# Performance work log

Hardware: AMD Instinct MI355X
Metric: run time of the kernel (lower is better)

## Reference

```python
import jax, jax.numpy as jnp
from jax import lax
import numpy as np

T, B, S, D, H, NC = 10, 16, 200, 768, 300, 4


def setup_inputs() -> dict:
    key = jax.random.key(0)
    ks = jax.random.split(key, 20)
    f = lambda k, shp: jax.random.normal(k, shp, dtype=jnp.float32)
    u = lambda k, shp: jax.random.uniform(k, shp, dtype=jnp.float32)
    return {
        "input_ids": jax.random.randint(ks[0], (B, T, 16), 0, 50265),
        "sequence_list": f(ks[1], (T, B, S, D)),
        "start_probs": u(ks[2], (T, B, S)),
        "end_probs": u(ks[3], (T, B, S)),
        "classification_probs": u(ks[4], (T, B, NC)),
        "before_state_start_probs": u(ks[5], (T, B, S)),
        "before_state_end_probs": u(ks[6], (T, B, S)),
        "before_state_classification_probs": u(ks[7], (T, B, NC)),
        "unk_mask": u(ks[8], (B, T, S)),
        "none_mask": u(ks[9], (B, T, S)),
        "ans_mask": u(ks[10], (B, T, S)),
        "Wih_f": f(ks[11], (4 * H, 5 * D)) * 0.02,
        "Whh_f": f(ks[12], (4 * H, H)) * 0.02,
        "bih_f": jnp.zeros((4 * H,), jnp.float32),
        "bhh_f": jnp.zeros((4 * H,), jnp.float32),
        "Wih_b": f(ks[13], (4 * H, 5 * D)) * 0.02,
        "Whh_b": f(ks[14], (4 * H, H)) * 0.02,
        "bih_b": jnp.zeros((4 * H,), jnp.float32),
        "bhh_b": jnp.zeros((4 * H,), jnp.float32),
        "Wcls": f(ks[15], (NC, S * 2 * H)) * 0.005,
        "bcls": jnp.zeros((NC,), jnp.float32),
    }


def _attn_weight(p, c, am, um, nm):
    # p: [B,S] probs; c: [B,NC] class probs; masks [B,S]
    # sum of three masked weighted copies collapses to one fused weight
    return p * (am * c[:, 0:1] + um * c[:, 1:2] + nm * c[:, 2:3])


def _lstm_dir(zx, Whh, bhh, h0, c0):
    # zx: [S,B,4H] precomputed x @ Wih.T + bih (big GEMM outside the scan)
    def step(carry, zt):
        h, c = carry
        z = zt + h @ Whh.T + bhh
        i, f, g, o = jnp.split(z, 4, axis=-1)  # torch gate order i,f,g,o
        c = jax.nn.sigmoid(f) * c + jax.nn.sigmoid(i) * jnp.tanh(g)
        h = jax.nn.sigmoid(o) * jnp.tanh(c)
        return (h, c), h
    (h, c), ys = lax.scan(step, (h0, c0), zx)
    return ys, h, c


def reference(input_ids, sequence_list, start_probs, end_probs, classification_probs,
              before_state_start_probs, before_state_end_probs, before_state_classification_probs,
              unk_mask, none_mask, ans_mask,
              Wih_f, Whh_f, bih_f, bhh_f, Wih_b, Whh_b, bih_b, bhh_b, Wcls, bcls):
    T_, B_, S_ = start_probs.shape
    H_ = Whh_f.shape[-1]
    amT = jnp.swapaxes(ans_mask, 0, 1)   # [T,B,S]
    umT = jnp.swapaxes(unk_mask, 0, 1)
    nmT = jnp.swapaxes(none_mask, 0, 1)
    # before-state attention (only step 0's probs are used, per the original code)
    bss = _attn_weight(before_state_start_probs[0], before_state_classification_probs[0],
                       amT[0], umT[0], nmT[0])[..., None] * sequence_list[0]
    bse = _attn_weight(before_state_end_probs[0], before_state_classification_probs[0],
                       amT[0], umT[0], nmT[0])[..., None] * sequence_list[0]
    z0 = jnp.zeros((B_, H_), start_probs.dtype)

    def outer(carry, xs):
        prev_s, prev_e, hf, cf, hb, cb = carry
        sp, ep, cp, am, um, nm, seq = xs
        s_att = _attn_weight(sp, cp, am, um, nm)[..., None] * seq  # [B,S,D]
        e_att = _attn_weight(ep, cp, am, um, nm)[..., None] * seq
        rnn_in = jnp.concatenate([seq, s_att, e_att, prev_s, prev_e], axis=-1)  # [B,S,5D]
        xT = jnp.swapaxes(rnn_in, 0, 1)  # [S,B,5D]
        zf = xT @ Wih_f.T + bih_f        # [S,B,4H]
        zb = xT[::-1] @ Wih_b.T + bih_b
        yf, hf, cf = _lstm_dir(zf, Whh_f, bhh_f, hf, cf)
        yb, hb, cb = _lstm_dir(zb, Whh_b, bhh_b, hb, cb)
        y = jnp.concatenate([yf, yb[::-1]], axis=-1)            # [S,B,2H]
        y = jnp.swapaxes(y, 0, 1).reshape(B_, -1)               # [B,S*2H]
        logits = jax.nn.relu(y) @ Wcls.T + bcls                 # [B,NC]
        return (s_att, e_att, hf, cf, hb, cb), logits

    init = (bss, bse, z0, z0, z0, z0)
    xs = (start_probs, end_probs, classification_probs, amT, umT, nmT, sequence_list)
    _, logits = lax.scan(outer, init, xs)
    return logits  # [T,B,NC]
```

## Files before the change

kernel.cpp:

```cpp
#include <hip/hip_runtime.h>
#include <stdint.h>
#include <stdio.h>

#define T_ 10
#define B_ 16
#define S_ 200
#define D_ 768
#define H_ 300
#define NC_ 4
#define M_ (S_ * B_)
#define K5_ (5 * D_)
#define N2_ 2400
#define G4_ 1200
#define HXW_SLOT 4864
#define HLDS_STRIDE 336

typedef unsigned short u16;
typedef unsigned int u32;
typedef __attribute__((ext_vector_type(8))) short short8;
typedef __attribute__((ext_vector_type(4))) float float4v;

static __device__ __forceinline__ u16 f2bf(float x) {
  union { float f; u32 u; } v; v.f = x;
  u32 u = v.u;
  u32 r = (u + 0x7FFFu + ((u >> 16) & 1u)) >> 16;
  return (u16)r;
}

static __device__ __forceinline__ void async16(const void* g, void* l) {
  __builtin_amdgcn_global_load_lds((const __attribute__((address_space(1))) u32*)g,
                                   (__attribute__((address_space(3))) u32*)l, 16, 0, 0);
}

static __device__ __forceinline__ float sigmoid_f(float x) {
  return 1.f / (1.f + __expf(-x));
}
static __device__ __forceinline__ float tanh_f(float x) {
  float e = __expf(2.f * x);
  return 1.f - 2.f / (e + 1.f);
}

__global__ void k_prep_s(const float* __restrict__ seq,
                         const float* __restrict__ sp, const float* __restrict__ ep,
                         const float* __restrict__ cp,
                         const float* __restrict__ bsp, const float* __restrict__ bep,
                         const float* __restrict__ bcp,
                         const float* __restrict__ um, const float* __restrict__ nm,
                         const float* __restrict__ am,
                         u16* __restrict__ s0, u16* __restrict__ sa, u16* __restrict__ sb,
                         u16* __restrict__ sa0, u16* __restrict__ sb0) {
  int bid = blockIdx.x;
  int tid = threadIdx.x;
  if (bid < T_ * M_) {
    int t = bid / M_;
    int r = bid % M_;
    int s = r >> 4, b = r & 15;
    float c0 = cp[(t * B_ + b) * NC_ + 0];
    float c1 = cp[(t * B_ + b) * NC_ + 1];
    float c2 = cp[(t * B_ + b) * NC_ + 2];
    int mi = (b * T_ + t) * S_ + s;
    float w = am[mi] * c0 + um[mi] * c1 + nm[mi] * c2;
    float aw = sp[(t * B_ + b) * S_ + s] * w;
    float bw = ep[(t * B_ + b) * S_ + s] * w;
    const float* x = seq + ((size_t)(t * B_ + b) * S_ + s) * D_;
    size_t ob = (size_t)bid * D_;
    for (int d = tid; d < D_; d += 256) {
      float xv = x[d];
      s0[ob + d] = f2bf(xv);
      sa[ob + d] = f2bf(aw * xv);
      sb[ob + d] = f2bf(bw * xv);
    }
  } else {
    int r = bid - T_ * M_;
    int s = r >> 4, b = r & 15;
    float c0 = bcp[b * NC_ + 0], c1 = bcp[b * NC_ + 1], c2 = bcp[b * NC_ + 2];
    int mi = (b * T_ + 0) * S_ + s;
    float w = am[mi] * c0 + um[mi] * c1 + nm[mi] * c2;
    float aw = bsp[b * S_ + s] * w;
    float bw = bep[b * S_ + s] * w;
    const float* x = seq + ((size_t)b * S_ + s) * D_;
    size_t ob = (size_t)r * D_;
    for (int d = tid; d < D_; d += 256) {
      float xv = x[d];
      sa0[ob + d] = f2bf(aw * xv);
      sb0[ob + d] = f2bf(bw * xv);
    }
  }
}

__global__ void k_prep_w(const float* __restrict__ wf, const float* __restrict__ wb,
                         const float* __restrict__ whf, const float* __restrict__ whb,
                         const float* __restrict__ bihf, const float* __restrict__ bhhf,
                         const float* __restrict__ bihb, const float* __restrict__ bhhb,
                         const float* __restrict__ bcls,
                         u16* __restrict__ wcat, u16* __restrict__ whh,
                         float* __restrict__ bias, float* __restrict__ outp,
                         u32* __restrict__ hxw) {
  int bid = blockIdx.x, tid = threadIdx.x;
  if (bid < N2_) {
    const float* src = bid < G4_ ? wf + (size_t)bid * K5_ : wb + (size_t)(bid - G4_) * K5_;
    u16* dst = wcat + (size_t)bid * K5_;
    for (int k = tid; k < K5_; k += 256) dst[k] = f2bf(src[k]);
  } else if (bid < N2_ + 2 * G4_) {
    int r = bid - N2_;
    int dir = r / G4_, n = r % G4_;
    const float* src = (dir ? whb : whf) + (size_t)n * H_;
    u16* dst = whh + (size_t)(dir * G4_ + n) * 320;
    for (int k = tid; k < 320; k += 256) dst[k] = (k < H_) ? f2bf(src[k]) : (u16)0;
  } else {
    for (int i = tid; i < 2 * G4_; i += 256) {
      int dir = i / G4_, n = i % G4_;
      bias[i] = dir ? (bihb[n] + bhhb[n]) : (bihf[n] + bhhf[n]);
    }
    for (int i = tid; i < T_ * B_ * NC_; i += 256) outp[i] = bcls[i & 3];
    for (int i = tid; i < 2 * 2 * HXW_SLOT; i += 256) hxw[i] = 0;
  }
}

__global__ __launch_bounds__(256, 3) void k_gemm(
    const u16* __restrict__ s0, const u16* __restrict__ sa, const u16* __restrict__ sb,
    const u16* __restrict__ sa0, const u16* __restrict__ sb0,
    const u16* __restrict__ wcat, float* __restrict__ z, int t) {
  __shared__ __align__(16) u16 As[128 * 32];
  __shared__ __align__(16) u16 Bs[128 * 32];
  int m0 = blockIdx.x * 128;
  int n0 = blockIdx.y * 128;
  int tid = threadIdx.x;
  int lane = tid & 63, wv = tid >> 6;
  int wm = wv & 1, wn = wv >> 1;

  const u16* ap[5];
  ap[0] = s0 + (size_t)t * M_ * D_;
  ap[1] = sa + (size_t)t * M_ * D_;
  ap[2] = sb + (size_t)t * M_ * D_;
  ap[3] = t ? sa + (size_t)(t - 1) * M_ * D_ : sa0;
  ap[4] = t ? sb + (size_t)(t - 1) * M_ * D_ : sb0;

  float4v acc[4][4];
#pragma unroll
  for (int i = 0; i < 4; i++)
#pragma unroll
    for (int j = 0; j < 4; j++) acc[i][j] = (float4v){0.f, 0.f, 0.f, 0.f};

  int rowA = tid >> 2;
  int seg = tid & 3;

  for (int which = 0; which < 5; ++which) {
    const u16* ab = which == 0 ? ap[0] : which == 1 ? ap[1] : which == 2 ? ap[2]
                    : which == 3 ? ap[3] : ap[4];
    for (int kk = 0; kk < 24; ++kk) {
      int kof = kk * 32;
#pragma unroll
      for (int j = 0; j < 2; ++j) {
        int row = j * 64 + rowA;
        const u16* g = ab + (size_t)(m0 + row) * D_ + kof + seg * 8;
        async16(g, As + wv * 512 + j * 2048);
      }
#pragma unroll
      for (int j = 0; j < 2; ++j) {
        int row = j * 64 + rowA;
        int nr = n0 + row;
        if (nr > N2_ - 1) nr = N2_ - 1;
        const u16* g = wcat + (size_t)nr * K5_ + which * D_ + kof + seg * 8;
        async16(g, Bs + wv * 512 + j * 2048);
      }
      __syncthreads();
      short8 af[4], bf[4];
#pragma unroll
      for (int i = 0; i < 4; i++) {
        af[i] = *(const short8*)&As[(wm * 64 + i * 16 + (lane & 15)) * 32 + (lane >> 4) * 8];
        bf[i] = *(const short8*)&Bs[(wn * 64 + i * 16 + (lane & 15)) * 32 + (lane >> 4) * 8];
      }
#pragma unroll
      for (int i = 0; i < 4; i++)
#pragma unroll
        for (int j = 0; j < 4; j++)
          acc[i][j] = __builtin_amdgcn_mfma_f32_16x16x32_bf16(af[i], bf[j], acc[i][j], 0, 0, 0);
      __syncthreads();
    }
  }
#pragma unroll
  for (int i = 0; i < 4; i++) {
    int m = m0 + wm * 64 + i * 16 + (lane >> 4) * 4;
#pragma unroll
    for (int j = 0; j < 4; j++) {
      int n = n0 + wn * 64 + j * 16 + (lane & 15);
      if (n < N2_) {
#pragma unroll
        for (int r = 0; r < 4; r++) z[(size_t)(m + r) * N2_ + n] = acc[i][j][r];
      }
    }
  }
}

__global__ __launch_bounds__(1024, 4) void k_lstm(
    const float* __restrict__ z, const u16* __restrict__ whh,
    const float* __restrict__ bias, const float* __restrict__ wcls,
    u32* __restrict__ hxw, float* __restrict__ outp,
    float* __restrict__ cst, int t) {
  __shared__ __align__(16) u16 h_lds[16 * HLDS_STRIDE];
  __shared__ __align__(16) float smem[4160];

  int wgid = blockIdx.x;
  int dir = wgid / 5;
  int w = wgid % 5;
  int tid = threadIdx.x;
  int lane = tid & 63, wv = tid >> 6;
  int gate = wv >> 2, q = wv & 3;

  short8 bfr[10];
  {
    int col = lane & 15;
    int u = w * 64 + q * 16 + col;
    int krow = (lane >> 4) * 8;
    if (u < H_) {
      const u16* base = whh + (size_t)(dir * G4_ + gate * H_ + u) * 320 + krow;
#pragma unroll
      for (int kk = 0; kk < 10; ++kk) bfr[kk] = *(const short8*)(base + kk * 32);
    } else {
#pragma unroll
      for (int kk = 0; kk < 10; ++kk) bfr[kk] = (short8){0, 0, 0, 0, 0, 0, 0, 0};
    }
  }

  int b = tid >> 6;
  int u_loc = tid & 63;
  int u_glob = w * 64 + u_loc;
  bool active = u_glob < H_;
  float bias_r[4];
#pragma unroll
  for (int g = 0; g < 4; ++g)
    bias_r[g] = active ? bias[dir * G4_ + g * H_ + u_glob] : 0.f;

  float c_state = t > 0 ? cst[wgid * 1024 + tid] : 0.f;
  float clsacc[4] = {0.f, 0.f, 0.f, 0.f};

  for (int i = tid; i < 16 * HLDS_STRIDE; i += 1024) h_lds[i] = 0;
  __syncthreads();

  u32* hx_base = hxw + dir * 2 * HXW_SLOT;

  u32 pend0 = 0, pendA = 0;
  int widx[5], lofs[5];
#pragma unroll
  for (int j = 0; j < 5; ++j) {
    int i = tid + j * 1024;
    widx[j] = i;
    lofs[j] = 0;
    if (i < 16 * 304) {
      int bb = i / 304;
      int uu = i - bb * 304;
      if (uu < H_) {
        lofs[j] = bb * HLDS_STRIDE + uu;
        pendA |= 1u << j;
        if (!(uu >= w * 64 && uu < (w + 1) * 64)) pend0 |= 1u << j;
      }
    }
  }

  for (int s_mod = 0; s_mod < S_; ++s_mod) {
    int g = t * S_ + s_mod;
    int s_in = dir ? (S_ - 1 - s_mod) : s_mod;

    float z_in[4] = {0.f, 0.f, 0.f, 0.f}, wc[4] = {0.f, 0.f, 0.f, 0.f};
    if (active) {
      const float* zr = z + (size_t)(s_in * B_ + b) * N2_ + dir * G4_;
      int ycol = s_in * 600 + dir * H_ + u_glob;
#pragma unroll
      for (int gg = 0; gg < 4; ++gg) z_in[gg] = zr[gg * H_ + u_glob];
#pragma unroll
      for (int n = 0; n < 4; ++n) wc[n] = wcls[(size_t)n * (S_ * 600) + ycol];
    }

    if (g > 0) {
      const u32* src = hx_base + (g & 1) * HXW_SLOT;
      u32 pend = (s_mod == 0) ? pendA : pend0;
      int tries = 0;
      while (pend && tries < (1 << 20)) {
        u32 got[5];
#pragma unroll
        for (int j = 0; j < 5; ++j)
          if (pend & (1u << j))
            got[j] = __hip_atomic_load(&src[widx[j]], __ATOMIC_RELAXED,
                                       __HIP_MEMORY_SCOPE_AGENT);
#pragma unroll
        for (int j = 0; j < 5; ++j)
          if ((pend & (1u << j)) && (got[j] >> 16) >= (u32)g) {
            h_lds[lofs[j]] = (u16)(got[j] & 0xffffu);
            pend &= ~(1u << j);
          }
        ++tries;
      }
      __syncthreads();
    }

    {
      float4v acc = (float4v){0.f, 0.f, 0.f, 0.f};
      int m = lane & 15;
      int kbase = (lane >> 4) * 8;
      const u16* hl = h_lds + m * HLDS_STRIDE + kbase;
#pragma unroll
      for (int kk = 0; kk < 10; ++kk) {
        short8 af = *(const short8*)(hl + kk * 32);
        acc = __builtin_amdgcn_mfma_f32_16x16x32_bf16(af, bfr[kk], acc, 0, 0, 0);
      }
      int col = lane & 15;
      int rb = (lane >> 4) * 4;
#pragma unroll
      for (int r = 0; r < 4; r++)
        smem[(gate * 16 + rb + r) * 65 + q * 16 + col] = acc[r];
    }
    __syncthreads();

    if (active) {
      float zi = smem[(0 * 16 + b) * 65 + u_loc] + z_in[0] + bias_r[0];
      float zf = smem[(1 * 16 + b) * 65 + u_loc] + z_in[1] + bias_r[1];
      float zg = smem[(2 * 16 + b) * 65 + u_loc] + z_in[2] + bias_r[2];
      float zo = smem[(3 * 16 + b) * 65 + u_loc] + z_in[3] + bias_r[3];
      float ig = sigmoid_f(zi);
      float fg = sigmoid_f(zf);
      float gg = tanh_f(zg);
      float og = sigmoid_f(zo);
      c_state = fg * c_state + ig * gg;
      float hval = og * tanh_f(c_state);
      u16 hb = f2bf(hval);
      u32 wrd = ((u32)(g + 1) << 16) | (u32)hb;
      __hip_atomic_store(&hx_base[((g + 1) & 1) * HXW_SLOT + b * 304 + u_glob], wrd,
                         __ATOMIC_RELAXED, __HIP_MEMORY_SCOPE_AGENT);
      h_lds[b * HLDS_STRIDE + u_glob] = hb;
      float rv = hval > 0.f ? hval : 0.f;
#pragma unroll
      for (int n = 0; n < 4; ++n) clsacc[n] += rv * wc[n];
    }

    if (s_mod == S_ - 1) {
      __syncthreads();
#pragma unroll
      for (int n = 0; n < 4; ++n) smem[(b * 64 + u_loc) * 4 + n] = clsacc[n];
      __syncthreads();
      if (tid < B_ * NC_) {
        int bb = tid >> 2, n = tid & 3;
        float s = 0.f;
        for (int u = 0; u < 64; ++u) s += smem[(bb * 64 + u) * 4 + n];
        atomicAdd(&outp[(t * B_ + bb) * NC_ + n], s);
      }
    }
  }
  cst[wgid * 1024 + tid] = c_state;
}

extern "C" void kernel_launch(void* const* d_in, const int* in_sizes, int n_in,
                              void* d_out, int out_size, void* d_ws, size_t ws_size,
                              hipStream_t stream) {
  const float* seq = (const float*)d_in[1];
  const float* sp = (const float*)d_in[2];
  const float* ep = (const float*)d_in[3];
  const float* cp = (const float*)d_in[4];
  const float* bsp = (const float*)d_in[5];
  const float* bep = (const float*)d_in[6];
  const float* bcp = (const float*)d_in[7];
  const float* um = (const float*)d_in[8];
  const float* nm = (const float*)d_in[9];
  const float* am = (const float*)d_in[10];
  const float* wihf = (const float*)d_in[11];
  const float* whhf = (const float*)d_in[12];
  const float* bihf = (const float*)d_in[13];
  const float* bhhf = (const float*)d_in[14];
  const float* wihb = (const float*)d_in[15];
  const float* whhb = (const float*)d_in[16];
  const float* bihb = (const float*)d_in[17];
  const float* bhhb = (const float*)d_in[18];
  const float* wcls = (const float*)d_in[19];
  const float* bcls = (const float*)d_in[20];

  char* ws = (char*)d_ws;
  size_t off = 0;
  auto alloc = [&](size_t bytes) -> char* {
    char* p = ws + off;
    off += (bytes + 255) & ~(size_t)255;
    return p;
  };
  u16* S0 = (u16*)alloc((size_t)T_ * M_ * D_ * 2);
  u16* SA = (u16*)alloc((size_t)T_ * M_ * D_ * 2);
  u16* SB = (u16*)alloc((size_t)T_ * M_ * D_ * 2);
  u16* SA0 = (u16*)alloc((size_t)M_ * D_ * 2);
  u16* SB0 = (u16*)alloc((size_t)M_ * D_ * 2);
  u16* WCAT = (u16*)alloc((size_t)N2_ * K5_ * 2);
  u16* WHH = (u16*)alloc((size_t)2 * G4_ * 320 * 2);
  float* BIAS = (float*)alloc((size_t)2 * G4_ * 4);
  float* Z = (float*)alloc((size_t)M_ * N2_ * 4);
  u32* HXW = (u32*)alloc((size_t)2 * 2 * HXW_SLOT * 4);
  float* CST = (float*)alloc((size_t)10 * 1024 * 4);

  if (off > ws_size) {
    fprintf(stderr, "[kernel] ws too small: need %zu, have %zu\n", off, ws_size);
    return;
  }

  hipLaunchKernelGGL(k_prep_s, dim3(T_ * M_ + M_), dim3(256), 0, stream,
                     seq, sp, ep, cp, bsp, bep, bcp, um, nm, am, S0, SA, SB, SA0, SB0);
  hipLaunchKernelGGL(k_prep_w, dim3(N2_ + 2 * G4_ + 1), dim3(256), 0, stream,
                     wihf, wihb, whhf, whhb, bihf, bhhf, bihb, bhhb, bcls,
                     WCAT, WHH, BIAS, (float*)d_out, HXW);
  for (int t = 0; t < T_; ++t) {
    hipLaunchKernelGGL(k_gemm, dim3(25, 19, 1), dim3(256), 0, stream,
                       S0, SA, SB, SA0, SB0, WCAT, Z, t);
    hipLaunchKernelGGL(k_lstm, dim3(10), dim3(1024), 0, stream,
                       Z, WHH, BIAS, wcls, HXW, (float*)d_out, CST, t);
  }
}
```

Baseline: 6.793 ms.

## Overlap next-step input GEMM with current LSTM recurrence in one fused launch

Merges the GEMM and LSTM kernels into one launch. The first 10 blocks run the recurrent LSTM for step t while the remaining 130 blocks compute the input projection GEMM for step t+1 into a double-buffered Z. The GEMM tile grows to 256x256 with 1024 threads. The LSTM polling loop now uses wide dwordx4 loads, and the h LDS stride is padded. This aims to hide the GEMM behind the latency-bound recurrence, at the cost of larger tiles and lower GEMM occupancy, and the GEMM blocks compete for bandwidth with the spinning LSTM blocks.

```diff
diff --git a/kernel.cpp b/kernel.cpp
--- a/kernel.cpp
+++ b/kernel.cpp
@@ -13,12 +13,13 @@
 #define N2_ 2400
 #define G4_ 1200
 #define HXW_SLOT 4864
-#define HLDS_STRIDE 336
+#define HLDS_STRIDE 344
 
 typedef unsigned short u16;
 typedef unsigned int u32;
 typedef __attribute__((ext_vector_type(8))) short short8;
 typedef __attribute__((ext_vector_type(4))) float float4v;
+typedef __attribute__((ext_vector_type(4))) unsigned int u32x4;
 
 static __device__ __forceinline__ u16 f2bf(float x) {
   union { float f; u32 u; } v; v.f = x;
@@ -117,96 +118,93 @@
   }
 }
 
-__global__ __launch_bounds__(256, 3) void k_gemm(
+__global__ __launch_bounds__(1024) void k_main(
     const u16* __restrict__ s0, const u16* __restrict__ sa, const u16* __restrict__ sb,
     const u16* __restrict__ sa0, const u16* __restrict__ sb0,
-    const u16* __restrict__ wcat, float* __restrict__ z, int t) {
-  __shared__ __align__(16) u16 As[128 * 32];
-  __shared__ __align__(16) u16 Bs[128 * 32];
-  int m0 = blockIdx.x * 128;
-  int n0 = blockIdx.y * 128;
+    const u16* __restrict__ wcat, float* __restrict__ zbase,
+    const u16* __restrict__ whh, const float* __restrict__ bias,
+    const float* __restrict__ wcls, u32* __restrict__ hxw,
+    float* __restrict__ outp, float* __restrict__ cst,
+    int t_lstm, int t_gemm, int nlstm) {
+  __shared__ __align__(16) char lds_raw[32768];
+
   int tid = threadIdx.x;
   int lane = tid & 63, wv = tid >> 6;
-  int wm = wv & 1, wn = wv >> 1;
-
-  const u16* ap[5];
-  ap[0] = s0 + (size_t)t * M_ * D_;
-  ap[1] = sa + (size_t)t * M_ * D_;
-  ap[2] = sb + (size_t)t * M_ * D_;
-  ap[3] = t ? sa + (size_t)(t - 1) * M_ * D_ : sa0;
-  ap[4] = t ? sb + (size_t)(t - 1) * M_ * D_ : sb0;
-
-  float4v acc[4][4];
-#pragma unroll
-  for (int i = 0; i < 4; i++)
-#pragma unroll
-    for (int j = 0; j < 4; j++) acc[i][j] = (float4v){0.f, 0.f, 0.f, 0.f};
-
-  int rowA = tid >> 2;
-  int seg = tid & 3;
-
-  for (int which = 0; which < 5; ++which) {
-    const u16* ab = which == 0 ? ap[0] : which == 1 ? ap[1] : which == 2 ? ap[2]
-                    : which == 3 ? ap[3] : ap[4];
-    for (int kk = 0; kk < 24; ++kk) {
-      int kof = kk * 32;
-#pragma unroll
-      for (int j = 0; j < 2; ++j) {
-        int row = j * 64 + rowA;
-        const u16* g = ab + (size_t)(m0 + row) * D_ + kof + seg * 8;
-        async16(g, As + wv * 512 + j * 2048);
-      }
-#pragma unroll
-      for (int j = 0; j < 2; ++j) {
-        int row = j * 64 + rowA;
-        int nr = n0 + row;
-        if (nr > N2_ - 1) nr = N2_ - 1;
-        const u16* g = wcat + (size_t)nr * K5_ + which * D_ + kof + seg * 8;
-        async16(g, Bs + wv * 512 + j * 2048);
-      }
-      __syncthreads();
-      short8 af[4], bf[4];
-#pragma unroll
-      for (int i = 0; i < 4; i++) {
-        af[i] = *(const short8*)&As[(wm * 64 + i * 16 + (lane & 15)) * 32 + (lane >> 4) * 8];
-        bf[i] = *(const short8*)&Bs[(wn * 64 + i * 16 + (lane & 15)) * 32 + (lane >> 4) * 8];
-      }
-#pragma unroll
-      for (int i = 0; i < 4; i++)
-#pragma unroll
-        for (int j = 0; j < 4; j++)
-          acc[i][j] = __builtin_amdgcn_mfma_f32_16x16x32_bf16(af[i], bf[j], acc[i][j], 0, 0, 0);
-      __syncthreads();
-    }
-  }
-#pragma unroll
-  for (int i = 0; i < 4; i++) {
-    int m = m0 + wm * 64 + i * 16 + (lane >> 4) * 4;
-#pragma unroll
-    for (int j = 0; j < 4; j++) {
-      int n = n0 + wn * 64 + j * 16 + (lane & 15);
-      if (n < N2_) {
-#pragma unroll
-        for (int r = 0; r < 4; r++) z[(size_t)(m + r) * N2_ + n] = acc[i][j][r];
-      }
-    }
-  }
-}
-
-__global__ __launch_bounds__(1024, 4) void k_lstm(
-    const float* __restrict__ z, const u16* __restrict__ whh,
-    const float* __restrict__ bias, const float* __restrict__ wcls,
-    u32* __restrict__ hxw, float* __restrict__ outp,
-    float* __restrict__ cst, int t) {
-  __shared__ __align__(16) u16 h_lds[16 * HLDS_STRIDE];
-  __shared__ __align__(16) float smem[4160];
-
+
+  if ((int)blockIdx.x >= nlstm) {
+    int bid = (int)blockIdx.x - nlstm;
+    int mt = bid % 13, nt = bid / 13;
+    int m0 = mt * 256, n0 = nt * 256;
+    u16* As = (u16*)lds_raw;
+    u16* Bs = (u16*)(lds_raw + 16384);
+    int wm = wv & 3, wn = wv >> 2;
+
+    const u16* ap[5];
+    ap[0] = s0 + (size_t)t_gemm * M_ * D_;
+    ap[1] = sa + (size_t)t_gemm * M_ * D_;
+    ap[2] = sb + (size_t)t_gemm * M_ * D_;
+    ap[3] = t_gemm ? sa + (size_t)(t_gemm - 1) * M_ * D_ : sa0;
+    ap[4] = t_gemm ? sb + (size_t)(t_gemm - 1) * M_ * D_ : sb0;
+    float* z = zbase + (size_t)(t_gemm & 1) * M_ * N2_;
+
+    float4v acc[4][4];
+#pragma unroll
+    for (int i = 0; i < 4; i++)
+#pragma unroll
+      for (int j = 0; j < 4; j++) acc[i][j] = (float4v){0.f, 0.f, 0.f, 0.f};
+
+    int rowA = tid >> 2;
+    int seg = tid & 3;
+    int mr = m0 + rowA; if (mr > M_ - 1) mr = M_ - 1;
+    int nr = n0 + rowA; if (nr > N2_ - 1) nr = N2_ - 1;
+
+    for (int which = 0; which < 5; ++which) {
+      const u16* ab = which == 0 ? ap[0] : which == 1 ? ap[1] : which == 2 ? ap[2]
+                      : which == 3 ? ap[3] : ap[4];
+      for (int kk = 0; kk < 24; ++kk) {
+        int kof = kk * 32;
+        async16(ab + (size_t)mr * D_ + kof + seg * 8, As + wv * 512);
+        async16(wcat + (size_t)nr * K5_ + which * D_ + kof + seg * 8, Bs + wv * 512);
+        __syncthreads();
+        short8 af[4], bf[4];
+#pragma unroll
+        for (int i = 0; i < 4; i++) {
+          af[i] = *(const short8*)&As[(wm * 64 + i * 16 + (lane & 15)) * 32 + (lane >> 4) * 8];
+          bf[i] = *(const short8*)&Bs[(wn * 64 + i * 16 + (lane & 15)) * 32 + (lane >> 4) * 8];
+        }
+#pragma unroll
+        for (int i = 0; i < 4; i++)
+#pragma unroll
+          for (int j = 0; j < 4; j++)
+            acc[i][j] = __builtin_amdgcn_mfma_f32_16x16x32_bf16(af[i], bf[j], acc[i][j], 0, 0, 0);
+        __syncthreads();
+      }
+    }
+#pragma unroll
+    for (int i = 0; i < 4; i++) {
+      int m = m0 + wm * 64 + i * 16 + (lane >> 4) * 4;
+#pragma unroll
+      for (int j = 0; j < 4; j++) {
+        int n = n0 + wn * 64 + j * 16 + (lane & 15);
+        if (n < N2_) {
+#pragma unroll
+          for (int r = 0; r < 4; r++)
+            if (m + r < M_) z[(size_t)(m + r) * N2_ + n] = acc[i][j][r];
+        }
+      }
+    }
+    return;
+  }
+
+  u16* h_lds = (u16*)lds_raw;
+  float* smem = (float*)(lds_raw + 16 * HLDS_STRIDE * 2);
+
+  int t = t_lstm;
   int wgid = blockIdx.x;
   int dir = wgid / 5;
   int w = wgid % 5;
-  int tid = threadIdx.x;
-  int lane = tid & 63, wv = tid >> 6;
   int gate = wv >> 2, q = wv & 3;
+  const float* z = zbase + (size_t)(t & 1) * M_ * N2_;
 
   short8 bfr[10];
   {
@@ -241,19 +239,18 @@
   u32* hx_base = hxw + dir * 2 * HXW_SLOT;
 
   u32 pend0 = 0, pendA = 0;
-  int widx[5], lofs[5];
-#pragma unroll
-  for (int j = 0; j < 5; ++j) {
-    int i = tid + j * 1024;
-    widx[j] = i;
-    lofs[j] = 0;
+  int lofs[8];
+#pragma unroll
+  for (int k = 0; k < 8; ++k) {
+    int i = (k < 4) ? (tid * 4 + k) : (4096 + tid * 4 + (k - 4));
+    lofs[k] = 0;
     if (i < 16 * 304) {
       int bb = i / 304;
       int uu = i - bb * 304;
       if (uu < H_) {
-        lofs[j] = bb * HLDS_STRIDE + uu;
-        pendA |= 1u << j;
-        if (!(uu >= w * 64 && uu < (w + 1) * 64)) pend0 |= 1u << j;
+        lofs[k] = bb * HLDS_STRIDE + uu;
+        pendA |= 1u << k;
+        if (!(uu >= w * 64 && uu < (w + 1) * 64)) pend0 |= 1u << k;
       }
     }
   }
@@ -274,20 +271,26 @@
 
     if (g > 0) {
       const u32* src = hx_base + (g & 1) * HXW_SLOT;
+      const u32* aA = src + tid * 4;
+      const u32* aB = src + 4096 + tid * 4;
       u32 pend = (s_mod == 0) ? pendA : pend0;
       int tries = 0;
       while (pend && tries < (1 << 20)) {
-        u32 got[5];
-#pragma unroll
-        for (int j = 0; j < 5; ++j)
-          if (pend & (1u << j))
-            got[j] = __hip_atomic_load(&src[widx[j]], __ATOMIC_RELAXED,
-                                       __HIP_MEMORY_SCOPE_AGENT);
-#pragma unroll
-        for (int j = 0; j < 5; ++j)
-          if ((pend & (1u << j)) && (got[j] >> 16) >= (u32)g) {
-            h_lds[lofs[j]] = (u16)(got[j] & 0xffffu);
-            pend &= ~(1u << j);
+        u32x4 gA, gB;
+        asm volatile(
+            "global_load_dwordx4 %0, %2, off sc0 sc1\n\t"
+            "global_load_dwordx4 %1, %3, off sc0 sc1\n\t"
+            "s_waitcnt vmcnt(0)"
+            : "=&v"(gA), "=&v"(gB)
+            : "v"(aA), "v"(aB)
+            : "memory");
+        __builtin_amdgcn_sched_barrier(0);
+        u32 wd[8] = {gA[0], gA[1], gA[2], gA[3], gB[0], gB[1], gB[2], gB[3]};
+#pragma unroll
+        for (int k = 0; k < 8; ++k)
+          if ((pend & (1u << k)) && (wd[k] >> 16) >= (u32)g) {
+            h_lds[lofs[k]] = (u16)(wd[k] & 0xffffu);
+            pend &= ~(1u << k);
           }
         ++tries;
       }
@@ -388,7 +391,7 @@
   u16* WCAT = (u16*)alloc((size_t)N2_ * K5_ * 2);
   u16* WHH = (u16*)alloc((size_t)2 * G4_ * 320 * 2);
   float* BIAS = (float*)alloc((size_t)2 * G4_ * 4);
-  float* Z = (float*)alloc((size_t)M_ * N2_ * 4);
+  float* Z = (float*)alloc((size_t)2 * M_ * N2_ * 4);
   u32* HXW = (u32*)alloc((size_t)2 * 2 * HXW_SLOT * 4);
   float* CST = (float*)alloc((size_t)10 * 1024 * 4);
 
@@ -402,10 +405,13 @@
   hipLaunchKernelGGL(k_prep_w, dim3(N2_ + 2 * G4_ + 1), dim3(256), 0, stream,
                      wihf, wihb, whhf, whhb, bihf, bhhf, bihb, bhhb, bcls,
                      WCAT, WHH, BIAS, (float*)d_out, HXW);
+  hipLaunchKernelGGL(k_main, dim3(130), dim3(1024), 0, stream,
+                     S0, SA, SB, SA0, SB0, WCAT, Z, WHH, BIAS, wcls, HXW,
+                     (float*)d_out, CST, 0, 0, 0);
   for (int t = 0; t < T_; ++t) {
-    hipLaunchKernelGGL(k_gemm, dim3(25, 19, 1), dim3(256), 0, stream,
-                       S0, SA, SB, SA0, SB0, WCAT, Z, t);
-    hipLaunchKernelGGL(k_lstm, dim3(10), dim3(1024), 0, stream,
-                       Z, WHH, BIAS, wcls, HXW, (float*)d_out, CST, t);
-  }
-}
+    int nb = (t < T_ - 1) ? 140 : 10;
+    hipLaunchKernelGGL(k_main, dim3(nb), dim3(1024), 0, stream,
+                       S0, SA, SB, SA0, SB0, WCAT, Z, WHH, BIAS, wcls, HXW,
+                       (float*)d_out, CST, t, t + 1, 10);
+  }
+}
```

Result: no change. 6.821 ms (+0.4%).
